# Optimization experiments

Hardware: AMD Instinct MI355X
Metric: run time of the kernel (lower is better)

## Reference

```python
import jax, jax.numpy as jnp
import numpy as np

B, L, D_IN, H, N, D_OUT = 32, 4096, 32, 256, 32, 16  # N = d_state//2 (conjugate pairs)


def setup_inputs() -> dict:
    key = jax.random.key(0)
    ks = jax.random.split(key, 16)
    s = lambda *sh: 1.0 / np.sqrt(sh[0])
    inp = {
        'data': jax.random.normal(ks[0], (B, L, D_IN), jnp.float32),
        # input projector: Linear(D_IN, H//2) -> ReLU -> Linear(H//2, H)
        'w1': jax.random.normal(ks[1], (D_IN, H // 2), jnp.float32) * s(D_IN),
        'b1': jnp.zeros((H // 2,), jnp.float32),
        'w2': jax.random.normal(ks[2], (H // 2, H), jnp.float32) * s(H // 2),
        'b2': jnp.zeros((H,), jnp.float32),
        # S4D diagonal SSM kernel params
        'log_dt': jax.random.uniform(ks[3], (H,), jnp.float32,
                                     np.log(0.001), np.log(0.1)),
        'A_re': -0.5 * jnp.ones((H, N), jnp.float32),
        'A_im': jnp.broadcast_to(np.pi * jnp.arange(N, dtype=jnp.float32), (H, N)),
        'C_re': jax.random.normal(ks[4], (H, N), jnp.float32) * s(2),
        'C_im': jax.random.normal(ks[5], (H, N), jnp.float32) * s(2),
        'D': jax.random.normal(ks[6], (H,), jnp.float32),
        # S4Block output position-wise linear H -> 2H with GLU
        'Wg': jax.random.normal(ks[7], (H, 2 * H), jnp.float32) * s(H),
        'bg': jnp.zeros((2 * H,), jnp.float32),
        # output projector: Linear(H, H//2) -> ReLU -> Linear(H//2, D_OUT)
        'w3': jax.random.normal(ks[8], (H, H // 2), jnp.float32) * s(H),
        'b3': jnp.zeros((H // 2,), jnp.float32),
        'w4': jax.random.normal(ks[9], (H // 2, D_OUT), jnp.float32) * s(H // 2),
        'b4': jnp.zeros((D_OUT,), jnp.float32),
    }
    return inp


def _s4_forward(data, w1, b1, w2, b2, log_dt, A_re, A_im, C_re, C_im, D,
                Wg, bg, w3, b3, w4, b4):
    # input projector (dropout disabled: eval mode)
    x = jnp.maximum(jnp.dot(data, w1) + b1, 0.0)
    x = jnp.dot(x, w2) + b2                      # (B, L, H)

    u = jnp.transpose(x, (0, 2, 1))              # (B, H, L)
    Lx = u.shape[-1]

    # S4D kernel: k[h,l] = 2 Re( sum_n C (e^{dtA}-1)/A * e^{dtA l} )
    dt = jnp.exp(log_dt)[:, None]                # (H, 1)
    A = A_re + 1j * A_im                         # (H, N)
    dtA = dt * A                                 # (H, N)
    C = C_re + 1j * C_im
    K_coef = C * (jnp.exp(dtA) - 1.0) / A        # (H, N)
    vand = jnp.exp(dtA[:, :, None] * jnp.arange(Lx))   # (H, N, L)
    k = 2.0 * jnp.einsum('hn,hnl->hl', K_coef, vand).real  # (H, L)

    # FFT convolution (causal, via 2L-point FFT) + skip D*u
    nfft = 2 * Lx
    kf = jnp.fft.rfft(k, nfft)                   # (H, nfft//2+1)
    uf = jnp.fft.rfft(u, nfft)                   # (B, H, nfft//2+1)
    y = jnp.fft.irfft(uf * kf[None], nfft)[..., :Lx] + D[None, :, None] * u

    y = jnp.transpose(y, (0, 2, 1))              # (B, L, H)
    y = jax.nn.gelu(y, approximate=False)

    # output linear with GLU
    y = jnp.dot(y, Wg) + bg                      # (B, L, 2H)
    a, b = jnp.split(y, 2, axis=-1)
    y = a * jax.nn.sigmoid(b)                    # (B, L, H)

    last = y[:, -1, :]                           # (B, H)
    z = jnp.maximum(jnp.dot(last, w3) + b3, 0.0)
    return jnp.dot(z, w4) + b4                   # (B, D_OUT); activ_type=None -> identity


def reference(data, w1, b1, w2, b2, log_dt, A_re, A_im, C_re, C_im, D,
              Wg, bg, w3, b3, w4, b4):
    return _s4_forward(data, w1, b1, w2, b2, log_dt, A_re, A_im, C_re, C_im, D,
                       Wg, bg, w3, b3, w4, b4)
```

## Files before the change

### kernel.cpp

```cpp
#include <hip/hip_runtime.h>
#include <math.h>


#define L_LEN 4096
#define H_DIM 256
#define J_DIM 128
#define DIN   32
#define NSTATE 32

typedef float f32x4 __attribute__((ext_vector_type(4)));
typedef short s16x8 __attribute__((ext_vector_type(8)));

__device__ __forceinline__ short f2bf(float x) {
  union { float f; unsigned u; } a; a.f = x;
  unsigned r = a.u + 0x7fffu + ((a.u >> 16) & 1u);
  return (short)(r >> 16);
}

__global__ __launch_bounds__(256) void k_prep(
    const float* __restrict__ w1, const float* __restrict__ w2,
    const float* __restrict__ log_dt,
    const float* __restrict__ A_re, const float* __restrict__ A_im,
    const float* __restrict__ C_re, const float* __restrict__ C_im,
    float* __restrict__ kkP,
    short* __restrict__ w1T, short* __restrict__ w2T)
{
  const int bid = blockIdx.x, tid = threadIdx.x;
  __shared__ float kcr[512], kci[512];

  {
    int i = bid * 256 + tid;
    if (i < 4096) {
      int n = i >> 5, k = i & 31;
      w1T[i] = f2bf(w1[k * J_DIM + n]);
    } else if (i < 36864) {
      int idx = i - 4096;
      int h = idx >> 7, k = idx & 127;
      w2T[idx] = f2bf(w2[k * H_DIM + h]);
    }
  }

  const int hg = bid >> 6, lcg = bid & 63;
  for (int e = tid; e < 512; e += 256) {
    int n = e & 31, h2 = e >> 5;
    int h = hg * 16 + h2;
    float dt = __expf(log_dt[h]);
    float are = A_re[h * NSTATE + n], aim = A_im[h * NSTATE + n];
    float dr = dt * are, di = dt * aim;
    float ed = __expf(dr);
    float c, s; __sincosf(di, &s, &c);
    float nr = ed * c - 1.f, ni = ed * s;
    float d2 = are * are + aim * aim;
    float qr = (nr * are + ni * aim) / d2;
    float qi = (ni * are - nr * aim) / d2;
    float cr = C_re[h * NSTATE + n], ci = C_im[h * NSTATE + n];
    kcr[n * 16 + h2] = cr * qr - ci * qi;
    kci[n * 16 + h2] = cr * qi + ci * qr;
  }
  __syncthreads();

  const int hh = tid & 15, lw = tid >> 4;
  const int h = hg * 16 + hh;
  const float dt = __expf(log_dt[h]);
  const float ar  = A_re[h * NSTATE];
  const float aib = A_im[h * NSTATE + 1];
#pragma unroll
  for (int it = 0; it < 4; it++) {
    int lc = lcg * 4 + it;
    int l = lc * 16 + lw;
    float fm = (float)((L_LEN - 1) - l);
    float mag = __expf(dt * ar * fm);
    float th = dt * aib * fm;
    float s1, c1; __sincosf(th, &s1, &c1);
    float cn = 1.f, sn = 0.f, acc = 0.f;
#pragma unroll
    for (int n = 0; n < NSTATE; n++) {
      acc += kcr[n * 16 + hh] * cn - kci[n * 16 + hh] * sn;
      float c2 = cn * c1 - sn * s1;
      sn = sn * c1 + cn * s1;
      cn = c2;
    }
    float val = 2.f * mag * acc;
    int c  = l >> 6, rt = (l >> 4) & 3, q = (l >> 2) & 3, r = l & 3;
    int w  = h >> 6, ht = (h >> 4) & 3, s15 = h & 15;
    kkP[((((c * 4 + w) * 4 + ht) * 4 + rt) * 64 + q * 16 + s15) * 4 + r] = val;
  }
}

__global__ __launch_bounds__(256) void k_main(
    const float* __restrict__ data, const float* __restrict__ b1v,
    const float* __restrict__ b2v, const float* __restrict__ Dv,
    const short* __restrict__ w1T, const short* __restrict__ w2T,
    const float* __restrict__ kkP, float* __restrict__ Pp)
{
  const int bidx = blockIdx.x, tid = threadIdx.x;
  const int wave = tid >> 6, lane = tid & 63;
  const int quad = lane >> 4, l15 = lane & 15;
  const int bp = bidx >> 6;
  const int lc = bidx & 63;
  const int l0 = lc * 64;

  __shared__ short x1s[2][64 * 136];

#pragma unroll
  for (int bb = 0; bb < 2; bb++) {
    const int b = bp * 2 + bb;
    const float* dp = data + ((size_t)b * L_LEN + (size_t)(l0 + wave * 16 + l15)) * DIN + quad * 8;
    f32x4 d0 = *(const f32x4*)dp;
    f32x4 d1 = *(const f32x4*)(dp + 4);
    s16x8 af;
    af[0] = f2bf(d0[0]); af[1] = f2bf(d0[1]); af[2] = f2bf(d0[2]); af[3] = f2bf(d0[3]);
    af[4] = f2bf(d1[0]); af[5] = f2bf(d1[1]); af[6] = f2bf(d1[2]); af[7] = f2bf(d1[3]);
#pragma unroll
    for (int c = 0; c < 8; c++) {
      s16x8 bf = *(const s16x8*)(w1T + (c * 16 + l15) * DIN + quad * 8);
      f32x4 a0 = {0.f, 0.f, 0.f, 0.f};
      a0 = __builtin_amdgcn_mfma_f32_16x16x32_bf16(af, bf, a0, 0, 0, 0);
      float bbi = b1v[c * 16 + l15];
#pragma unroll
      for (int r = 0; r < 4; r++) {
        float v = fmaxf(a0[r] + bbi, 0.f);
        x1s[bb][(wave * 16 + quad * 4 + r) * 136 + c * 16 + l15] = f2bf(v);
      }
    }
  }

  s16x8 wf[4][4];
#pragma unroll
  for (int ht = 0; ht < 4; ht++)
#pragma unroll
    for (int ks = 0; ks < 4; ks++)
      wf[ht][ks] = *(const s16x8*)(w2T + (wave * 64 + ht * 16 + l15) * J_DIM + ks * 32 + quad * 8);

  __syncthreads();

#pragma unroll 1
  for (int bb = 0; bb < 2; bb++) {
    const int b = bp * 2 + bb;

    f32x4 acc[4][4];
#pragma unroll
    for (int rt = 0; rt < 4; rt++)
#pragma unroll
      for (int ht = 0; ht < 4; ht++)
        acc[rt][ht] = (f32x4){0.f, 0.f, 0.f, 0.f};

#pragma unroll
    for (int ks = 0; ks < 4; ks++) {
#pragma unroll
      for (int rt = 0; rt < 4; rt++) {
        s16x8 af = *(const s16x8*)&x1s[bb][(rt * 16 + l15) * 136 + ks * 32 + quad * 8];
#pragma unroll
        for (int ht = 0; ht < 4; ht++)
          acc[rt][ht] = __builtin_amdgcn_mfma_f32_16x16x32_bf16(af, wf[ht][ks], acc[rt][ht], 0, 0, 0);
      }
    }

#pragma unroll
    for (int ht = 0; ht < 4; ht++) {
      int h = wave * 64 + ht * 16 + l15;
      float b2h = b2v[h], Dh = Dv[h];
      const f32x4* kp = ((const f32x4*)kkP)
                      + (((lc * 4 + wave) * 4 + ht) * 4) * 64 + lane;
      float s = 0.f;
#pragma unroll
      for (int rt = 0; rt < 4; rt++) {
        f32x4 kv = kp[rt * 64];
#pragma unroll
        for (int r = 0; r < 4; r++) {
          int l = l0 + rt * 16 + quad * 4 + r;
          float uu = acc[rt][ht][r] + b2h;
          s = fmaf(kv[r], uu, s);
          if (l == L_LEN - 1) s = fmaf(Dh, uu, s);
        }
      }
      s += __shfl_xor(s, 16, 64);
      s += __shfl_xor(s, 32, 64);
      if (quad == 0) Pp[(size_t)(lc * 32 + b) * H_DIM + h] = s;
    }
  }
}

__global__ __launch_bounds__(1024) void k_tail(
    const float* __restrict__ Pp, const float* __restrict__ Wg,
    const float* __restrict__ bgv, const float* __restrict__ w3,
    const float* __restrict__ b3v, const float* __restrict__ w4,
    const float* __restrict__ b4v, float* __restrict__ out)
{
  const int b = blockIdx.x, t = threadIdx.x;
  __shared__ float pp[4][H_DIM];
  __shared__ float g[H_DIM];
  __shared__ float part[2][512];
  __shared__ float glu[H_DIM];
  __shared__ float zp[8][J_DIM];
  __shared__ float zf[J_DIM];

  {
    int h = t & 255, kc = t >> 8;
    float s = 0.f;
#pragma unroll
    for (int i = 0; i < 16; i++)
      s += Pp[(size_t)((kc * 16 + i) * 32 + b) * H_DIM + h];
    pp[kc][h] = s;
  }
  __syncthreads();
  if (t < H_DIM) {
    float p = pp[0][t] + pp[1][t] + pp[2][t] + pp[3][t];
    g[t] = 0.5f * p * (1.f + erff(p * 0.70710678118654752f));
  }
  __syncthreads();

  {
    int col = t & 511, kc = t >> 9;
    const float* wp = Wg + (size_t)(kc * 128) * 512 + col;
    float acc = 0.f;
#pragma unroll 16
    for (int j = 0; j < 128; j++)
      acc = fmaf(g[kc * 128 + j], wp[(size_t)j * 512], acc);
    part[kc][col] = acc;
  }
  __syncthreads();
  if (t < 512) part[0][t] = bgv[t] + part[0][t] + part[1][t];
  __syncthreads();
  if (t < H_DIM)
    glu[t] = part[0][t] * (1.f / (1.f + expf(-part[0][H_DIM + t])));
  __syncthreads();

  {
    int col = t & 127, kc = t >> 7;
    const float* wp = w3 + (size_t)(kc * 32) * J_DIM + col;
    float acc = 0.f;
#pragma unroll
    for (int j = 0; j < 32; j++)
      acc = fmaf(glu[kc * 32 + j], wp[(size_t)j * J_DIM], acc);
    zp[kc][col] = acc;
  }
  __syncthreads();
  if (t < J_DIM) {
    float s = b3v[t];
#pragma unroll
    for (int k = 0; k < 8; k++) s += zp[k][t];
    zf[t] = fmaxf(s, 0.f);
  }
  __syncthreads();

  if (t < 16) {
    float s = b4v[t];
#pragma unroll
    for (int i = 0; i < J_DIM; i++)
      s = fmaf(zf[i], w4[i * 16 + t], s);
    out[b * 16 + t] = s;
  }
}

extern "C" void kernel_launch(void* const* d_in, const int* in_sizes, int n_in,
                              void* d_out, int out_size, void* d_ws, size_t ws_size,
                              hipStream_t stream)
{
  const float* data   = (const float*)d_in[0];
  const float* w1     = (const float*)d_in[1];
  const float* b1v    = (const float*)d_in[2];
  const float* w2     = (const float*)d_in[3];
  const float* b2v    = (const float*)d_in[4];
  const float* log_dt = (const float*)d_in[5];
  const float* A_re   = (const float*)d_in[6];
  const float* A_im   = (const float*)d_in[7];
  const float* C_re   = (const float*)d_in[8];
  const float* C_im   = (const float*)d_in[9];
  const float* Dv     = (const float*)d_in[10];
  const float* Wg     = (const float*)d_in[11];
  const float* bgv    = (const float*)d_in[12];
  const float* w3     = (const float*)d_in[13];
  const float* b3v    = (const float*)d_in[14];
  const float* w4     = (const float*)d_in[15];
  const float* b4v    = (const float*)d_in[16];
  float* outp = (float*)d_out;

  char* ws = (char*)d_ws;
  float* kkP = (float*)ws;
  float* Pp  = (float*)(ws + 4194304);
  short* w1T = (short*)(ws + 4194304 + 2097152);
  short* w2T = (short*)(ws + 4194304 + 2097152 + 8192);

  k_prep<<<1024, 256, 0, stream>>>(w1, w2, log_dt, A_re, A_im, C_re, C_im,
                                   kkP, w1T, w2T);
  k_main<<<1024, 256, 0, stream>>>(data, b1v, b2v, Dv, w1T, w2T, kkP, Pp);
  k_tail<<<32, 1024, 0, stream>>>(Pp, Wg, bgv, w3, b3v, w4, b4v, outp);
}
```

Before: 134.6 us.

## Split k_main h-tiles into two passes to cut registers and raise occupancy

The second GEMM in k_main now handles its four h-tiles in two passes of two. Each pass reloads the w2 fragments and prefetches the kernel values before the MFMA loop. This shrinks the live weight and accumulator register set, and launch_bounds now requests 3 blocks per SM to raise occupancy. In exchange, w2 fragments are reloaded once per batch element instead of being held across both, which adds global/L2 traffic and instructions.

Measured after the change: 146.4 us. +8.8%, slower.

```diff
diff --git a/kernel.cpp b/kernel.cpp
--- a/kernel.cpp
+++ b/kernel.cpp
@@ -87,7 +87,7 @@
   }
 }
 
-__global__ __launch_bounds__(256) void k_main(
+__global__ __launch_bounds__(256, 3) void k_main(
     const float* __restrict__ data, const float* __restrict__ b1v,
     const float* __restrict__ b2v, const float* __restrict__ Dv,
     const short* __restrict__ w1T, const short* __restrict__ w2T,
@@ -125,58 +125,68 @@
     }
   }
 
-  s16x8 wf[4][4];
-#pragma unroll
-  for (int ht = 0; ht < 4; ht++)
-#pragma unroll
-    for (int ks = 0; ks < 4; ks++)
-      wf[ht][ks] = *(const s16x8*)(w2T + (wave * 64 + ht * 16 + l15) * J_DIM + ks * 32 + quad * 8);
-
   __syncthreads();
 
 #pragma unroll 1
   for (int bb = 0; bb < 2; bb++) {
     const int b = bp * 2 + bb;
 
-    f32x4 acc[4][4];
-#pragma unroll
-    for (int rt = 0; rt < 4; rt++)
-#pragma unroll
-      for (int ht = 0; ht < 4; ht++)
-        acc[rt][ht] = (f32x4){0.f, 0.f, 0.f, 0.f};
-
-#pragma unroll
-    for (int ks = 0; ks < 4; ks++) {
-#pragma unroll
-      for (int rt = 0; rt < 4; rt++) {
-        s16x8 af = *(const s16x8*)&x1s[bb][(rt * 16 + l15) * 136 + ks * 32 + quad * 8];
-#pragma unroll
-        for (int ht = 0; ht < 4; ht++)
-          acc[rt][ht] = __builtin_amdgcn_mfma_f32_16x16x32_bf16(af, wf[ht][ks], acc[rt][ht], 0, 0, 0);
-      }
-    }
-
-#pragma unroll
-    for (int ht = 0; ht < 4; ht++) {
-      int h = wave * 64 + ht * 16 + l15;
-      float b2h = b2v[h], Dh = Dv[h];
-      const f32x4* kp = ((const f32x4*)kkP)
-                      + (((lc * 4 + wave) * 4 + ht) * 4) * 64 + lane;
-      float s = 0.f;
-#pragma unroll
-      for (int rt = 0; rt < 4; rt++) {
-        f32x4 kv = kp[rt * 64];
-#pragma unroll
-        for (int r = 0; r < 4; r++) {
-          int l = l0 + rt * 16 + quad * 4 + r;
-          float uu = acc[rt][ht][r] + b2h;
-          s = fmaf(kv[r], uu, s);
-          if (l == L_LEN - 1) s = fmaf(Dh, uu, s);
+#pragma unroll 1
+    for (int hp = 0; hp < 2; hp++) {
+      s16x8 wf2[2][4];
+#pragma unroll
+      for (int h2 = 0; h2 < 2; h2++)
+#pragma unroll
+        for (int ks = 0; ks < 4; ks++)
+          wf2[h2][ks] = *(const s16x8*)(w2T + (wave * 64 + (hp * 2 + h2) * 16 + l15) * J_DIM + ks * 32 + quad * 8);
+
+      const f32x4* kpB = ((const f32x4*)kkP)
+                       + (((lc * 4 + wave) * 4 + hp * 2) * 4) * 64 + lane;
+      f32x4 kv[2][4];
+#pragma unroll
+      for (int h2 = 0; h2 < 2; h2++)
+#pragma unroll
+        for (int rt = 0; rt < 4; rt++)
+          kv[h2][rt] = kpB[h2 * 256 + rt * 64];
+
+      f32x4 acc2[4][2];
+#pragma unroll
+      for (int rt = 0; rt < 4; rt++)
+#pragma unroll
+        for (int h2 = 0; h2 < 2; h2++)
+          acc2[rt][h2] = (f32x4){0.f, 0.f, 0.f, 0.f};
+
+#pragma unroll
+      for (int ks = 0; ks < 4; ks++) {
+#pragma unroll
+        for (int rt = 0; rt < 4; rt++) {
+          s16x8 af = *(const s16x8*)&x1s[bb][(rt * 16 + l15) * 136 + ks * 32 + quad * 8];
+#pragma unroll
+          for (int h2 = 0; h2 < 2; h2++)
+            acc2[rt][h2] = __builtin_amdgcn_mfma_f32_16x16x32_bf16(af, wf2[h2][ks], acc2[rt][h2], 0, 0, 0);
         }
       }
-      s += __shfl_xor(s, 16, 64);
-      s += __shfl_xor(s, 32, 64);
-      if (quad == 0) Pp[(size_t)(lc * 32 + b) * H_DIM + h] = s;
+
+#pragma unroll
+      for (int h2 = 0; h2 < 2; h2++) {
+        int ht = hp * 2 + h2;
+        int h = wave * 64 + ht * 16 + l15;
+        float b2h = b2v[h], Dh = Dv[h];
+        float s = 0.f;
+#pragma unroll
+        for (int rt = 0; rt < 4; rt++) {
+#pragma unroll
+          for (int r = 0; r < 4; r++) {
+            int l = l0 + rt * 16 + quad * 4 + r;
+            float uu = acc2[rt][h2][r] + b2h;
+            s = fmaf(kv[h2][rt][r], uu, s);
+            if (l == L_LEN - 1) s = fmaf(Dh, uu, s);
+          }
+        }
+        s += __shfl_xor(s, 16, 64);
+        s += __shfl_xor(s, 32, 64);
+        if (quad == 0) Pp[(size_t)(lc * 32 + b) * H_DIM + h] = s;
+      }
     }
   }
 }
```

## Keep first-layer MFMA output in registers and shrink k_main tiles

Applied to the files above, without the earlier changes.

Pre-permutes w1 and w2 into MFMA fragment order so the first-layer MFMA is computed transposed. Its accumulator outputs then map directly to the A-fragment of the second MFMA, which removes the LDS staging buffer and the __syncthreads. Each block now handles 16 sequence positions instead of 64, and the grid grows to 4096 blocks for more parallelism. The cost is four times more partial-sum rows in Pp for k_tail to reduce, plus weights reloaded per block.

New measurement: 153.8 us. 14.2% more time.

```diff
diff --git a/kernel.cpp b/kernel.cpp
--- a/kernel.cpp
+++ b/kernel.cpp
@@ -23,7 +23,7 @@
     const float* __restrict__ A_re, const float* __restrict__ A_im,
     const float* __restrict__ C_re, const float* __restrict__ C_im,
     float* __restrict__ kkP,
-    short* __restrict__ w1T, short* __restrict__ w2T)
+    short* __restrict__ w1P, short* __restrict__ w2P)
 {
   const int bid = blockIdx.x, tid = threadIdx.x;
   __shared__ float kcr[512], kci[512];
@@ -31,12 +31,15 @@
   {
     int i = bid * 256 + tid;
     if (i < 4096) {
-      int n = i >> 5, k = i & 31;
-      w1T[i] = f2bf(w1[k * J_DIM + n]);
+      int s = i & 7, Lr = (i >> 3) & 63, c = i >> 9;
+      int k = ((Lr >> 4) << 3) + s, j = c * 16 + (Lr & 15);
+      w1P[i] = f2bf(w1[k * J_DIM + j]);
     } else if (i < 36864) {
-      int idx = i - 4096;
-      int h = idx >> 7, k = idx & 127;
-      w2T[idx] = f2bf(w2[k * H_DIM + h]);
+      int i2 = i - 4096;
+      int s = i2 & 7, M = (i2 >> 3) & 63, ks = (i2 >> 9) & 3, T = i2 >> 11;
+      int j = (2 * ks + (s >> 2)) * 16 + ((M >> 4) << 2) + (s & 3);
+      int h = T * 16 + (M & 15);
+      w2P[i2] = f2bf(w2[j * H_DIM + h]);
     }
   }
 
@@ -90,93 +93,88 @@
 __global__ __launch_bounds__(256) void k_main(
     const float* __restrict__ data, const float* __restrict__ b1v,
     const float* __restrict__ b2v, const float* __restrict__ Dv,
-    const short* __restrict__ w1T, const short* __restrict__ w2T,
+    const short* __restrict__ w1P, const short* __restrict__ w2P,
     const float* __restrict__ kkP, float* __restrict__ Pp)
 {
   const int bidx = blockIdx.x, tid = threadIdx.x;
   const int wave = tid >> 6, lane = tid & 63;
-  const int quad = lane >> 4, l15 = lane & 15;
-  const int bp = bidx >> 6;
-  const int lc = bidx & 63;
-  const int l0 = lc * 64;
-
-  __shared__ short x1s[2][64 * 136];
-
-#pragma unroll
-  for (int bb = 0; bb < 2; bb++) {
-    const int b = bp * 2 + bb;
-    const float* dp = data + ((size_t)b * L_LEN + (size_t)(l0 + wave * 16 + l15)) * DIN + quad * 8;
-    f32x4 d0 = *(const f32x4*)dp;
-    f32x4 d1 = *(const f32x4*)(dp + 4);
-    s16x8 af;
-    af[0] = f2bf(d0[0]); af[1] = f2bf(d0[1]); af[2] = f2bf(d0[2]); af[3] = f2bf(d0[3]);
-    af[4] = f2bf(d1[0]); af[5] = f2bf(d1[1]); af[6] = f2bf(d1[2]); af[7] = f2bf(d1[3]);
-#pragma unroll
-    for (int c = 0; c < 8; c++) {
-      s16x8 bf = *(const s16x8*)(w1T + (c * 16 + l15) * DIN + quad * 8);
-      f32x4 a0 = {0.f, 0.f, 0.f, 0.f};
-      a0 = __builtin_amdgcn_mfma_f32_16x16x32_bf16(af, bf, a0, 0, 0, 0);
-      float bbi = b1v[c * 16 + l15];
-#pragma unroll
-      for (int r = 0; r < 4; r++) {
-        float v = fmaxf(a0[r] + bbi, 0.f);
-        x1s[bb][(wave * 16 + quad * 4 + r) * 136 + c * 16 + l15] = f2bf(v);
-      }
-    }
-  }
-
-  s16x8 wf[4][4];
+  const int q = lane >> 4, l15 = lane & 15;
+  const int lt = bidx & 255;
+  const int bp = bidx >> 8;
+  const int Q = wave;
+
+  s16x8 w1f[8];
+#pragma unroll
+  for (int c = 0; c < 8; c++)
+    w1f[c] = *(const s16x8*)(w1P + (c * 64 + lane) * 8);
+
+  s16x8 wk[4][4];
 #pragma unroll
   for (int ht = 0; ht < 4; ht++)
 #pragma unroll
     for (int ks = 0; ks < 4; ks++)
-      wf[ht][ks] = *(const s16x8*)(w2T + (wave * 64 + ht * 16 + l15) * J_DIM + ks * 32 + quad * 8);
-
-  __syncthreads();
+      wk[ht][ks] = *(const s16x8*)(w2P + (((Q * 4 + ht) * 4 + ks) * 64 + lane) * 8);
+
+  const int c_l = lt >> 2, rt = lt & 3;
+  f32x4 kv[4];
+  float b2h[4], Dh[4];
+#pragma unroll
+  for (int ht = 0; ht < 4; ht++) {
+    kv[ht] = *((const f32x4*)kkP + ((((c_l * 4 + Q) * 4 + ht) * 4 + rt) * 64 + lane));
+    int h = Q * 64 + ht * 16 + l15;
+    b2h[ht] = b2v[h]; Dh[ht] = Dv[h];
+  }
 
 #pragma unroll 1
   for (int bb = 0; bb < 2; bb++) {
     const int b = bp * 2 + bb;
 
-    f32x4 acc[4][4];
-#pragma unroll
-    for (int rt = 0; rt < 4; rt++)
+    const float* dp = data + ((size_t)b * L_LEN + (size_t)(lt * 16 + l15)) * DIN + q * 8;
+    f32x4 d0 = *(const f32x4*)dp;
+    f32x4 d1 = *(const f32x4*)(dp + 4);
+    s16x8 db;
+    db[0] = f2bf(d0[0]); db[1] = f2bf(d0[1]); db[2] = f2bf(d0[2]); db[3] = f2bf(d0[3]);
+    db[4] = f2bf(d1[0]); db[5] = f2bf(d1[1]); db[6] = f2bf(d1[2]); db[7] = f2bf(d1[3]);
+
+    f32x4 pa[8];
+#pragma unroll
+    for (int c = 0; c < 8; c++) {
+      f32x4 bi = *(const f32x4*)(b1v + c * 16 + q * 4);
+      pa[c] = __builtin_amdgcn_mfma_f32_16x16x32_bf16(w1f[c], db, bi, 0, 0, 0);
+    }
+
+    s16x8 af[4];
+#pragma unroll
+    for (int ks = 0; ks < 4; ks++) {
+#pragma unroll
+      for (int s = 0; s < 8; s++) {
+        af[ks][s] = f2bf(fmaxf(pa[2 * ks + (s >> 2)][s & 3], 0.f));
+      }
+    }
+
+    f32x4 acc[4];
+#pragma unroll
+    for (int ht = 0; ht < 4; ht++)
+      acc[ht] = (f32x4){0.f, 0.f, 0.f, 0.f};
+#pragma unroll
+    for (int ks = 0; ks < 4; ks++)
 #pragma unroll
       for (int ht = 0; ht < 4; ht++)
-        acc[rt][ht] = (f32x4){0.f, 0.f, 0.f, 0.f};
-
-#pragma unroll
-    for (int ks = 0; ks < 4; ks++) {
-#pragma unroll
-      for (int rt = 0; rt < 4; rt++) {
-        s16x8 af = *(const s16x8*)&x1s[bb][(rt * 16 + l15) * 136 + ks * 32 + quad * 8];
-#pragma unroll
-        for (int ht = 0; ht < 4; ht++)
-          acc[rt][ht] = __builtin_amdgcn_mfma_f32_16x16x32_bf16(af, wf[ht][ks], acc[rt][ht], 0, 0, 0);
-      }
-    }
+        acc[ht] = __builtin_amdgcn_mfma_f32_16x16x32_bf16(af[ks], wk[ht][ks], acc[ht], 0, 0, 0);
 
 #pragma unroll
     for (int ht = 0; ht < 4; ht++) {
-      int h = wave * 64 + ht * 16 + l15;
-      float b2h = b2v[h], Dh = Dv[h];
-      const f32x4* kp = ((const f32x4*)kkP)
-                      + (((lc * 4 + wave) * 4 + ht) * 4) * 64 + lane;
       float s = 0.f;
 #pragma unroll
-      for (int rt = 0; rt < 4; rt++) {
-        f32x4 kv = kp[rt * 64];
-#pragma unroll
-        for (int r = 0; r < 4; r++) {
-          int l = l0 + rt * 16 + quad * 4 + r;
-          float uu = acc[rt][ht][r] + b2h;
-          s = fmaf(kv[r], uu, s);
-          if (l == L_LEN - 1) s = fmaf(Dh, uu, s);
-        }
+      for (int r = 0; r < 4; r++) {
+        int l = lt * 16 + q * 4 + r;
+        float uu = acc[ht][r] + b2h[ht];
+        s = fmaf(kv[ht][r], uu, s);
+        if (l == L_LEN - 1) s = fmaf(Dh[ht], uu, s);
       }
       s += __shfl_xor(s, 16, 64);
       s += __shfl_xor(s, 32, 64);
-      if (quad == 0) Pp[(size_t)(lc * 32 + b) * H_DIM + h] = s;
+      if (q == 0) Pp[(size_t)(lt * 32 + b) * H_DIM + Q * 64 + ht * 16 + l15] = s;
     }
   }
 }
@@ -198,9 +196,9 @@
   {
     int h = t & 255, kc = t >> 8;
     float s = 0.f;
-#pragma unroll
-    for (int i = 0; i < 16; i++)
-      s += Pp[(size_t)((kc * 16 + i) * 32 + b) * H_DIM + h];
+#pragma unroll 8
+    for (int i = 0; i < 64; i++)
+      s += Pp[(size_t)((kc * 64 + i) * 32 + b) * H_DIM + h];
     pp[kc][h] = s;
   }
   __syncthreads();
@@ -279,11 +277,11 @@
   char* ws = (char*)d_ws;
   float* kkP = (float*)ws;
   float* Pp  = (float*)(ws + 4194304);
-  short* w1T = (short*)(ws + 4194304 + 2097152);
-  short* w2T = (short*)(ws + 4194304 + 2097152 + 8192);
+  short* w1P = (short*)(ws + 4194304 + 8388608);
+  short* w2P = (short*)(ws + 4194304 + 8388608 + 8192);
 
   k_prep<<<1024, 256, 0, stream>>>(w1, w2, log_dt, A_re, A_im, C_re, C_im,
-                                   kkP, w1T, w2T);
-  k_main<<<1024, 256, 0, stream>>>(data, b1v, b2v, Dv, w1T, w2T, kkP, Pp);
+                                   kkP, w1P, w2P);
+  k_main<<<4096, 256, 0, stream>>>(data, b1v, b2v, Dv, w1P, w2P, kkP, Pp);
   k_tail<<<32, 1024, 0, stream>>>(Pp, Wg, bgv, w3, b3v, w4, b4v, outp);
 }
```

## Split tail into reduction, GLU-GEMV and final kernels with transposed Wg

Applied to the files above, without the earlier changes.

The single 32-block tail kernel is replaced by three kernels. The first reduces the partial sums and applies GELU. The second computes the Wg projection across 64 blocks, with one wave per output column pair, pairing the GLU gate through a shuffle. The third runs the small output MLP. The prep kernel now also transposes Wg so the GEMV reads contiguous rows. The aim is to spread the Wg reads (512 KB of weights, read once per batch item) over more CUs than the 32 blocks used before, at the cost of two extra launches and global round trips for the intermediates.

After: 147.0 us. 1.09x slower.

```diff
diff --git a/kernel.cpp b/kernel.cpp
--- a/kernel.cpp
+++ b/kernel.cpp
@@ -19,11 +19,13 @@
 
 __global__ __launch_bounds__(256) void k_prep(
     const float* __restrict__ w1, const float* __restrict__ w2,
+    const float* __restrict__ Wg,
     const float* __restrict__ log_dt,
     const float* __restrict__ A_re, const float* __restrict__ A_im,
     const float* __restrict__ C_re, const float* __restrict__ C_im,
     float* __restrict__ kkP,
-    short* __restrict__ w1T, short* __restrict__ w2T)
+    short* __restrict__ w1T, short* __restrict__ w2T,
+    float* __restrict__ WgT)
 {
   const int bid = blockIdx.x, tid = threadIdx.x;
   __shared__ float kcr[512], kci[512];
@@ -37,6 +39,10 @@
       int idx = i - 4096;
       int h = idx >> 7, k = idx & 127;
       w2T[idx] = f2bf(w2[k * H_DIM + h]);
+    } else if (i < 167936) {
+      int idx = i - 36864;
+      int c = idx >> 8, j = idx & 255;
+      WgT[idx] = Wg[(size_t)j * 512 + c];
     }
   }
 
@@ -181,49 +187,51 @@
   }
 }
 
-__global__ __launch_bounds__(1024) void k_tail(
-    const float* __restrict__ Pp, const float* __restrict__ Wg,
-    const float* __restrict__ bgv, const float* __restrict__ w3,
+__global__ __launch_bounds__(128) void k_act(
+    const float* __restrict__ Pp, float* __restrict__ g)
+{
+  int idx = blockIdx.x * 128 + threadIdx.x;
+  int h = idx & 255, b = idx >> 8;
+  float s = 0.f;
+#pragma unroll 8
+  for (int i = 0; i < 64; i++)
+    s += Pp[(size_t)(i * 32 + b) * H_DIM + h];
+  g[b * H_DIM + h] = 0.5f * s * (1.f + erff(s * 0.70710678118654752f));
+}
+
+__global__ __launch_bounds__(256) void k_glu(
+    const float* __restrict__ g, const float* __restrict__ WgT,
+    const float* __restrict__ bgv, float* __restrict__ glu)
+{
+  const int wave = threadIdx.x >> 6, lane = threadIdx.x & 63;
+  const int p = blockIdx.x * 4 + wave;
+  const int b = lane & 31, half = lane >> 5;
+  const int col = p + half * 256;
+  const float* wrow = WgT + (size_t)col * 256;
+  const float* grow = g + b * 256;
+  float acc = 0.f;
+#pragma unroll 8
+  for (int j = 0; j < 256; j++)
+    acc = fmaf(grow[j], wrow[j], acc);
+  acc += bgv[col];
+  float other = __shfl(acc, lane + 32, 64);
+  if (half == 0) {
+    float sig = 1.f / (1.f + __expf(-other));
+    glu[b * 256 + p] = acc * sig;
+  }
+}
+
+__global__ __launch_bounds__(1024) void k_fin(
+    const float* __restrict__ glu, const float* __restrict__ w3,
     const float* __restrict__ b3v, const float* __restrict__ w4,
     const float* __restrict__ b4v, float* __restrict__ out)
 {
   const int b = blockIdx.x, t = threadIdx.x;
-  __shared__ float pp[4][H_DIM];
-  __shared__ float g[H_DIM];
-  __shared__ float part[2][512];
-  __shared__ float glu[H_DIM];
+  __shared__ float gl[H_DIM];
   __shared__ float zp[8][J_DIM];
   __shared__ float zf[J_DIM];
 
-  {
-    int h = t & 255, kc = t >> 8;
-    float s = 0.f;
-#pragma unroll
-    for (int i = 0; i < 16; i++)
-      s += Pp[(size_t)((kc * 16 + i) * 32 + b) * H_DIM + h];
-    pp[kc][h] = s;
-  }
-  __syncthreads();
-  if (t < H_DIM) {
-    float p = pp[0][t] + pp[1][t] + pp[2][t] + pp[3][t];
-    g[t] = 0.5f * p * (1.f + erff(p * 0.70710678118654752f));
-  }
-  __syncthreads();
-
-  {
-    int col = t & 511, kc = t >> 9;
-    const float* wp = Wg + (size_t)(kc * 128) * 512 + col;
-    float acc = 0.f;
-#pragma unroll 16
-    for (int j = 0; j < 128; j++)
-      acc = fmaf(g[kc * 128 + j], wp[(size_t)j * 512], acc);
-    part[kc][col] = acc;
-  }
-  __syncthreads();
-  if (t < 512) part[0][t] = bgv[t] + part[0][t] + part[1][t];
-  __syncthreads();
-  if (t < H_DIM)
-    glu[t] = part[0][t] * (1.f / (1.f + expf(-part[0][H_DIM + t])));
+  if (t < H_DIM) gl[t] = glu[b * H_DIM + t];
   __syncthreads();
 
   {
@@ -232,7 +240,7 @@
     float acc = 0.f;
 #pragma unroll
     for (int j = 0; j < 32; j++)
-      acc = fmaf(glu[kc * 32 + j], wp[(size_t)j * J_DIM], acc);
+      acc = fmaf(gl[kc * 32 + j], wp[(size_t)j * J_DIM], acc);
     zp[kc][col] = acc;
   }
   __syncthreads();
@@ -279,11 +287,16 @@
   char* ws = (char*)d_ws;
   float* kkP = (float*)ws;
   float* Pp  = (float*)(ws + 4194304);
-  short* w1T = (short*)(ws + 4194304 + 2097152);
-  short* w2T = (short*)(ws + 4194304 + 2097152 + 8192);
-
-  k_prep<<<1024, 256, 0, stream>>>(w1, w2, log_dt, A_re, A_im, C_re, C_im,
-                                   kkP, w1T, w2T);
+  short* w1T = (short*)(ws + 6291456);
+  short* w2T = (short*)(ws + 6299648);
+  float* WgT = (float*)(ws + 6365184);
+  float* g   = (float*)(ws + 6889472);
+  float* glu = (float*)(ws + 6922240);
+
+  k_prep<<<1024, 256, 0, stream>>>(w1, w2, Wg, log_dt, A_re, A_im, C_re, C_im,
+                                   kkP, w1T, w2T, WgT);
   k_main<<<1024, 256, 0, stream>>>(data, b1v, b2v, Dv, w1T, w2T, kkP, Pp);
-  k_tail<<<32, 1024, 0, stream>>>(Pp, Wg, bgv, w3, b3v, w4, b4v, outp);
-}
+  k_act<<<64, 128, 0, stream>>>(Pp, g);
+  k_glu<<<64, 256, 0, stream>>>(g, WgT, bgv, glu);
+  k_fin<<<32, 1024, 0, stream>>>(glu, w3, b3v, w4, b4v, outp);
+}
```
